# Performance work log

Measured on AMD Instinct MI355X. Metric: run time of the kernel, lower is better.

## Reference

```python
import jax, jax.numpy as jnp
import numpy as np

B, S, CL, DIM, HEADS, FFN = 2, 2048, 512, 2048, 16, 8192
EPS = 1e-6


def rms_norm(x, w):
    return x * jax.lax.rsqrt(jnp.mean(x * x, axis=-1, keepdims=True) + EPS) * w


def mha(q, k, v, num_heads):
    b, sq, d = q.shape
    sk = k.shape[1]
    hd = d // num_heads
    q = q.reshape(b, sq, num_heads, hd)
    k = k.reshape(b, sk, num_heads, hd)
    v = v.reshape(b, sk, num_heads, hd)
    attn = jnp.einsum('bqhd,bkhd->bhqk', q, k) * (hd ** -0.5)
    attn = jax.nn.softmax(attn, axis=-1)
    out = jnp.einsum('bhqk,bkhd->bqhd', attn, v)
    return out.reshape(b, sq, d)


def setup_inputs() -> dict:
    key = jax.random.key(0)
    ks = iter(jax.random.split(key, 48))
    nrm = lambda shape, scale: jax.random.normal(next(ks), shape, jnp.float32) * scale
    w_scale = DIM ** -0.5
    inp = {
        'x': nrm((B, S, DIM), 1.0),
        'e': nrm((B, 6, DIM), 0.5),
        'context': nrm((B, CL, DIM), 1.0),
        'modulation': nrm((1, 6, DIM), w_scale),
        'norm1_w': jnp.ones((DIM,), jnp.float32),
        'norm2_w': jnp.ones((DIM,), jnp.float32),
        'norm3_w': jnp.ones((DIM,), jnp.float32),
        'sa_nq_w': jnp.ones((DIM,), jnp.float32),
        'sa_nk_w': jnp.ones((DIM,), jnp.float32),
        'ffn_norm_w': jnp.ones((DIM,), jnp.float32),
        'sa_qw': nrm((DIM, DIM), w_scale), 'sa_qb': jnp.zeros((DIM,), jnp.float32),
        'sa_kw': nrm((DIM, DIM), w_scale), 'sa_kb': jnp.zeros((DIM,), jnp.float32),
        'sa_vw': nrm((DIM, DIM), w_scale), 'sa_vb': jnp.zeros((DIM,), jnp.float32),
        'sa_ow': nrm((DIM, DIM), w_scale), 'sa_ob': jnp.zeros((DIM,), jnp.float32),
        'ca_qw': nrm((DIM, DIM), w_scale), 'ca_qb': jnp.zeros((DIM,), jnp.float32),
        'ca_kw': nrm((DIM, DIM), w_scale), 'ca_kb': jnp.zeros((DIM,), jnp.float32),
        'ca_vw': nrm((DIM, DIM), w_scale), 'ca_vb': jnp.zeros((DIM,), jnp.float32),
        'ca_ow': nrm((DIM, DIM), w_scale), 'ca_ob': jnp.zeros((DIM,), jnp.float32),
        'ffn_w1': nrm((DIM, FFN), w_scale), 'ffn_b1': jnp.zeros((FFN,), jnp.float32),
        'ffn_w2': nrm((FFN, DIM), FFN ** -0.5), 'ffn_b2': jnp.zeros((DIM,), jnp.float32),
    }
    return inp


def reference(x, e, context, modulation, norm1_w, norm2_w, norm3_w, sa_nq_w, sa_nk_w,
              ffn_norm_w, sa_qw, sa_qb, sa_kw, sa_kb, sa_vw, sa_vb, sa_ow, sa_ob,
              ca_qw, ca_qb, ca_kw, ca_kb, ca_vw, ca_vb, ca_ow, ca_ob,
              ffn_w1, ffn_b1, ffn_w2, ffn_b2):
    # AdaLN modulation: (modulation + e) chunked into 6 along dim=1 -> each [B,1,DIM]
    mod = modulation + e
    e0, e1, e2, e3, e4, e5 = [mod[:, i:i + 1, :] for i in range(6)]

    # --- self attention with qk_norm=True ---
    h = rms_norm(x, norm1_w) * (1.0 + e1) + e0
    q = rms_norm(h @ sa_qw + sa_qb, sa_nq_w)
    k = rms_norm(h @ sa_kw + sa_kb, sa_nk_w)
    v = h @ sa_vw + sa_vb
    y = mha(q, k, v, HEADS) @ sa_ow + sa_ob
    x = x + y * e2

    # --- cross attention (cross_attn_norm=False, no qk norm) ---
    h = rms_norm(x, norm2_w)
    q = h @ ca_qw + ca_qb
    k = context @ ca_kw + ca_kb
    v = context @ ca_vw + ca_vb
    y = mha(q, k, v, HEADS) @ ca_ow + ca_ob
    x = x + y

    # --- FFN: modulate(norm3(x)) -> RMSNorm -> Linear -> GELU(tanh) -> Linear ---
    h = rms_norm(x, norm3_w) * (1.0 + e4) + e3
    h = rms_norm(h, ffn_norm_w)
    h = jax.nn.gelu(h @ ffn_w1 + ffn_b1, approximate=True)
    y = h @ ffn_w2 + ffn_b2
    x = x + y * e5
    return x
```

## Files before the change

### kernel.cpp

```cpp
#include <hip/hip_runtime.h>
#include <hip/hip_bf16.h>
#include <cstdint>

#define DIM   2048
#define HEADS 16
#define HD    128
#define SEQ   2048
#define CLEN  512
#define FFND  8192
#define BATCH 2

using bf16 = __hip_bfloat16;
typedef __attribute__((ext_vector_type(8))) short  short8;
typedef __attribute__((ext_vector_type(4))) short  short4v;
typedef __attribute__((ext_vector_type(4))) float  f32x4;
typedef __attribute__((ext_vector_type(8))) __bf16 bf16x8;

__device__ __forceinline__ short f2bs(float f){ bf16 h = __float2bfloat16(f); return __builtin_bit_cast(short, h); }
__device__ __forceinline__ float bs2f(short s){ return __builtin_bit_cast(float, (uint32_t)((uint16_t)s) << 16); }

__device__ __forceinline__ f32x4 mfma16(short8 a, short8 b, f32x4 c){
  return __builtin_amdgcn_mfma_f32_16x16x32_bf16(
      __builtin_bit_cast(bf16x8, a), __builtin_bit_cast(bf16x8, b), c, 0, 0, 0);
}

__device__ __forceinline__ void gload_lds16(const void* g, const void* l){
  __builtin_amdgcn_global_load_lds(
      (const __attribute__((address_space(1))) void*)(uintptr_t)g,
      (__attribute__((address_space(3))) void*)(uint32_t)(uintptr_t)l, 16, 0, 0);
}

__device__ __forceinline__ float block_sum(float v, float* sbuf, int tid){
  #pragma unroll
  for (int m = 32; m >= 1; m >>= 1) v += __shfl_xor(v, m, 64);
  const int w = tid >> 6;
  if ((tid & 63) == 0) sbuf[w] = v;
  __syncthreads();
  float r = sbuf[0] + sbuf[1] + sbuf[2] + sbuf[3];
  __syncthreads();
  return r;
}


__global__ void modadd_k(const float* __restrict__ m, const float* __restrict__ e,
                         float* __restrict__ out){
  int i = blockIdx.x * 256 + threadIdx.x;
  out[i] = m[i % (6 * DIM)] + e[i];
}

__global__ void f2b8_k(const float* __restrict__ in, bf16* __restrict__ out){
  int i = blockIdx.x * 256 + threadIdx.x;
  const float4* p = (const float4*)in;
  float4 a = p[2*i], c = p[2*i+1];
  short8 o;
  o[0]=f2bs(a.x); o[1]=f2bs(a.y); o[2]=f2bs(a.z); o[3]=f2bs(a.w);
  o[4]=f2bs(c.x); o[5]=f2bs(c.y); o[6]=f2bs(c.z); o[7]=f2bs(c.w);
  *((short8*)out + i) = o;
}

__global__ void biascat_k(const float* __restrict__ b0, const float* __restrict__ b1,
                          const float* __restrict__ b2, float* __restrict__ bcat){
  int i = blockIdx.x * 256 + threadIdx.x;
  const float* src = (i < DIM) ? b0 : (i < 2*DIM) ? b1 : b2;
  bcat[i] = src[i & (DIM-1)];
}

__global__ __launch_bounds__(256) void transpose_w(const float* __restrict__ W,
                                                   bf16* __restrict__ Wt, int K, int N){
  __shared__ float tile[32][33];
  const int tx = threadIdx.x & 31, ty = threadIdx.x >> 5;
  const size_t k0 = blockIdx.y * 32, n0 = blockIdx.x * 32;
  #pragma unroll
  for (int i = 0; i < 4; i++)
    tile[ty + i*8][tx] = W[(k0 + ty + i*8) * (size_t)N + n0 + tx];
  __syncthreads();
  #pragma unroll
  for (int i = 0; i < 4; i++)
    Wt[(n0 + ty + i*8) * (size_t)K + k0 + tx] = __float2bfloat16(tile[tx][ty + i*8]);
}

template<int MODE>
__global__ __launch_bounds__(256) void norm_x(const float* __restrict__ x,
    const float* __restrict__ w1, const float* __restrict__ w2,
    const float* __restrict__ mod, bf16* __restrict__ out, int S)
{
  const int row = blockIdx.x, tid = threadIdx.x;
  const int b = row / S;
  __shared__ float sbuf[4];
  const float* xr = x + (size_t)row * DIM;
  float v[8];
  #pragma unroll
  for (int i = 0; i < 2; i++){
    float4 t = *(const float4*)(xr + i*1024 + tid*4);
    v[i*4+0]=t.x; v[i*4+1]=t.y; v[i*4+2]=t.z; v[i*4+3]=t.w;
  }
  float ss = 0.f;
  #pragma unroll
  for (int j = 0; j < 8; j++) ss += v[j]*v[j];
  ss = block_sum(ss, sbuf, tid);
  const float r = rsqrtf(ss * (1.0f/DIM) + 1e-6f);
  const float* mb = mod + (size_t)b * 6 * DIM;
  float t8[8];
  #pragma unroll
  for (int i = 0; i < 2; i++)
    #pragma unroll
    for (int j = 0; j < 4; j++){
      int n = i*1024 + tid*4 + j;
      float val = v[i*4+j] * r * w1[n];
      if (MODE == 1) val = val * (1.f + mb[DIM + n]) + mb[n];
      if (MODE == 3) val = val * (1.f + mb[4*DIM + n]) + mb[3*DIM + n];
      t8[i*4+j] = val;
    }
  if (MODE == 3){
    float s2 = 0.f;
    #pragma unroll
    for (int j = 0; j < 8; j++) s2 += t8[j]*t8[j];
    s2 = block_sum(s2, sbuf, tid);
    const float r2 = rsqrtf(s2 * (1.0f/DIM) + 1e-6f);
    #pragma unroll
    for (int i = 0; i < 2; i++)
      #pragma unroll
      for (int j = 0; j < 4; j++){
        int n = i*1024 + tid*4 + j;
        t8[i*4+j] = t8[i*4+j] * r2 * w2[n];
      }
  }
  #pragma unroll
  for (int i = 0; i < 2; i++){
    short4v o;
    #pragma unroll
    for (int j = 0; j < 4; j++) o[j] = f2bs(t8[i*4+j]);
    *(short4v*)(out + (size_t)row*DIM + i*1024 + tid*4) = o;
  }
}

__global__ __launch_bounds__(256) void rmsnorm_bf16_ip(bf16* __restrict__ x,
                                                       const float* __restrict__ w){
  const int row = blockIdx.x, tid = threadIdx.x;
  __shared__ float sbuf[4];
  bf16* xr = x + (size_t)row * DIM;
  short8 v = *(const short8*)(xr + tid*8);
  float f[8]; float ss = 0.f;
  #pragma unroll
  for (int j = 0; j < 8; j++){ f[j] = bs2f(v[j]); ss += f[j]*f[j]; }
  ss = block_sum(ss, sbuf, tid);
  const float r = rsqrtf(ss * (1.0f/DIM) + 1e-6f);
  short8 o;
  #pragma unroll
  for (int j = 0; j < 8; j++) o[j] = f2bs(f[j] * r * w[tid*8 + j]);
  *(short8*)(xr + tid*8) = o;
}

template<int WM, int EPI>
__global__ __launch_bounds__(512) void gemm_v10(
    const bf16* __restrict__ A, const bf16* __restrict__ Bt,
    const float* __restrict__ bias, const float* __restrict__ xin,
    const float* __restrict__ mod, float* __restrict__ outf,
    bf16* __restrict__ outb, bf16* __restrict__ out1, bf16* __restrict__ out2,
    int M, int N, int K, int S_tok, int eidx)
{
  constexpr int WN  = 8 / WM;
  constexpr int BN  = WN * 64;
  constexpr int RPW = 256 / WM;
  constexpr int MI  = RPW / 16;
  constexpr int PH  = MI / 2;
  constexpr int ABYTES = 256 * 64 * 2;
  constexpr int BBYTES = BN * 64 * 2;
  constexpr int NBJ = BBYTES / 8192;

  __shared__ __align__(16) char lds[2][ABYTES + BBYTES];

  const int tid = threadIdx.x;
  const int w = tid >> 6, l = tid & 63;
  const int lrow = l & 15, lhi = l >> 4;
  const int wr = w / WN, wc = w % WN;
  const size_t m0 = (size_t)blockIdx.y * 256, n0 = (size_t)blockIdx.x * BN;

  f32x4 acc[MI][4] = {};

  const int srow = tid >> 3;
  const int sseg = (tid & 7) ^ (srow & 7);
  const bf16* gA[4]; const bf16* gB[NBJ];
  #pragma unroll
  for (int j = 0; j < 4; j++)   gA[j] = A  + (m0 + srow + 64*j) * (size_t)K + sseg*8;
  #pragma unroll
  for (int j = 0; j < NBJ; j++) gB[j] = Bt + (n0 + srow + 64*j) * (size_t)K + sseg*8;

  const int nt = K >> 6;

  {
    char* buf = lds[0];
    #pragma unroll
    for (int j = 0; j < 4; j++)   gload_lds16(gA[j], buf + (tid + j*512)*16);
    #pragma unroll
    for (int j = 0; j < NBJ; j++) gload_lds16(gB[j], buf + ABYTES + (tid + j*512)*16);
  }
  asm volatile("s_waitcnt vmcnt(0)" ::: "memory");
  __builtin_amdgcn_s_barrier();

  for (int t = 0; t < nt; ++t){
    const char* br = lds[t & 1];
    char* sb = lds[(t + 1) & 1];
    const bool dost = (t + 1 < nt);
    const size_t ko = (size_t)(t + 1) * 64;
    short8 bf[4];
    #pragma unroll
    for (int p = 0; p < PH; ++p){
      const int ks  = (MI == 8) ? (p >> 1) : p;
      const int mi0 = (MI == 8) ? (p & 1) * 4 : 0;
      const int seg = ((ks*4 + lhi) ^ (lrow & 7)) * 16;
      short8 af[4];
      #pragma unroll
      for (int i = 0; i < 4; i++){
        const int row = wr*RPW + (mi0 + i)*16 + lrow;
        af[i] = *(const short8*)(br + row*128 + seg);
      }
      if (MI == 4 || (p & 1) == 0){
        #pragma unroll
        for (int ni = 0; ni < 4; ni++){
          const int row = wc*64 + ni*16 + lrow;
          bf[ni] = *(const short8*)(br + ABYTES + row*128 + seg);
        }
      }
      if (dost){
        if (MI == 8){
          if (p == 0){
            #pragma unroll
            for (int j = 0; j < 4; j++)   gload_lds16(gA[j] + ko, sb + (tid + j*512)*16);
          } else if (p == 1){
            #pragma unroll
            for (int j = 0; j < NBJ; j++) gload_lds16(gB[j] + ko, sb + ABYTES + (tid + j*512)*16);
          }
        } else {
          if (p == 0){
            #pragma unroll
            for (int j = 0; j < 4; j++)   gload_lds16(gA[j] + ko, sb + (tid + j*512)*16);
            #pragma unroll
            for (int j = 0; j < NBJ; j++) gload_lds16(gB[j] + ko, sb + ABYTES + (tid + j*512)*16);
          }
        }
      }
      __builtin_amdgcn_sched_barrier(0);
      __builtin_amdgcn_s_barrier();
      asm volatile("s_waitcnt lgkmcnt(0)" ::: "memory");
      __builtin_amdgcn_sched_barrier(0);
      __builtin_amdgcn_s_setprio(1);
      #pragma unroll
      for (int i = 0; i < 4; i++)
        #pragma unroll
        for (int ni = 0; ni < 4; ni++)
          acc[mi0 + i][ni] = mfma16(af[i], bf[ni], acc[mi0 + i][ni]);
      __builtin_amdgcn_s_setprio(0);
      if (p == PH - 1){ asm volatile("s_waitcnt vmcnt(0)" ::: "memory"); }
      __builtin_amdgcn_sched_barrier(0);
      __builtin_amdgcn_s_barrier();
    }
  }

  #pragma unroll
  for (int mi = 0; mi < MI; mi++)
    #pragma unroll
    for (int ni = 0; ni < 4; ni++)
      #pragma unroll
      for (int r = 0; r < 4; r++){
        const size_t m = m0 + wr*RPW + mi*16 + lhi*4 + r;
        const size_t n = n0 + wc*64 + ni*16 + lrow;
        float v = acc[mi][ni][r] + bias[n];
        if constexpr (EPI == 0) {
          outb[m * N + n] = __float2bfloat16(v);
        } else if constexpr (EPI == 1) {
          const size_t b = m / S_tok, s = m % S_tok;
          const size_t h = n >> 7, d = n & 127;
          outb[((b*HEADS + h)*HD + d) * S_tok + s] = __float2bfloat16(v);
        } else if constexpr (EPI == 2) {
          const float ev = mod[(m / S_tok) * 6 * DIM + (size_t)eidx * DIM + n];
          outf[m * N + n] = xin[m * N + n] + v * ev;
        } else if constexpr (EPI == 3) {
          outf[m * N + n] += v;
        } else if constexpr (EPI == 4) {
          float u = 0.7978845608028654f * (v + 0.044715f * v * v * v);
          outb[m * N + n] = __float2bfloat16(0.5f * v * (1.0f + tanhf(u)));
        } else {
          const size_t sg = n >> 11, col = n & 2047;
          if (sg == 0)      outb[m * DIM + col] = __float2bfloat16(v);
          else if (sg == 1) out1[m * DIM + col] = __float2bfloat16(v);
          else {
            const size_t b = m / S_tok, s = m % S_tok;
            const size_t h = col >> 7, d = col & 127;
            out2[((b*HEADS + h)*HD + d) * S_tok + s] = __float2bfloat16(v);
          }
        }
      }
}

__global__ __launch_bounds__(256, 2) void attn_fwd(
    const bf16* __restrict__ Q, const bf16* __restrict__ Kp, const bf16* __restrict__ Vt,
    bf16* __restrict__ O, int SQ, int SKV)
{
  const int tid = threadIdx.x, w = tid >> 6, l = tid & 63;
  const int lrow = l & 15, lhi = l >> 4;
  const int nwg = gridDim.x;
  const int p = blockIdx.x;
  const int f = (p & 7) * (nwg >> 3) + (p >> 3);
  const int nqb = SQ >> 6;
  const int xq = f % nqb;
  const int h  = (f / nqb) % HEADS;
  const int b  = f / (nqb * HEADS);
  const int q0 = xq * 64 + w * 16;

  __shared__ __align__(16) char kls[2][16384];
  __shared__ __align__(16) char vls[2][16384];
  __shared__ __align__(16) bf16 P[4][16][72];
  const float scale = 0.08838834764831845f;

  const bf16* qp = Q + ((size_t)(b*SQ + q0 + lrow))*DIM + h*HD + lhi*8;
  short8 qf[4];
  #pragma unroll
  for (int ds = 0; ds < 4; ds++) qf[ds] = *(const short8*)(qp + ds*32);

  const bf16* kg = Kp + (size_t)b*SKV*DIM + h*HD;
  const bf16* vg = Vt + (size_t)(b*HEADS + h)*HD*SKV;

  f32x4 acc[8] = {};
  float m_run = -INFINITY, l_run = 0.f;
  const int nt = SKV >> 6;

  auto stage = [&](int buf, int kv0){
    char* kd = &kls[buf][0];
    #pragma unroll
    for (int i = 0; i < 4; i++){
      int sid = i*256 + tid;
      int row = sid >> 4, sg = sid & 15;
      int gsg = sg ^ (row & 7);
      gload_lds16(kg + (size_t)(kv0 + row)*DIM + gsg*8, kd + sid*16);
    }
    char* vd = &vls[buf][0];
    #pragma unroll
    for (int i = 0; i < 4; i++){
      int sid = i*256 + tid;
      int d = sid >> 3, sg = sid & 7;
      int gsg = sg ^ (d & 7);
      gload_lds16(vg + (size_t)d*SKV + kv0 + gsg*8, vd + sid*16);
    }
  };

  stage(0, 0);
  __syncthreads();

  for (int t = 0; t < nt; ++t){
    if (t + 1 < nt) stage((t + 1) & 1, (t + 1) * 64);
    const char* kb = &kls[t & 1][0];
    const char* vb = &vls[t & 1][0];

    f32x4 st[4] = {};
    #pragma unroll
    for (int kvf = 0; kvf < 4; kvf++){
      const int row = kvf*16 + lrow;
      const int rx = row & 7;
      #pragma unroll
      for (int ds = 0; ds < 4; ds++){
        const int seg = (ds*4 + lhi) ^ rx;
        short8 kf = *(const short8*)(kb + row*256 + seg*16);
        st[kvf] = mfma16(kf, qf[ds], st[kvf]);
      }
    }

    float sv[16]; float smax = -INFINITY;
    #pragma unroll
    for (int kvf = 0; kvf < 4; kvf++)
      #pragma unroll
      for (int r = 0; r < 4; r++){
        float xv = st[kvf][r] * scale;
        sv[kvf*4+r] = xv; smax = fmaxf(smax, xv);
      }
    smax = fmaxf(smax, __shfl_xor(smax, 16, 64));
    smax = fmaxf(smax, __shfl_xor(smax, 32, 64));
    const float mnew = fmaxf(m_run, smax);
    const float corr = __expf(m_run - mnew);
    float psum = 0.f;
    #pragma unroll
    for (int i = 0; i < 16; i++){ float pe = __expf(sv[i] - mnew); sv[i] = pe; psum += pe; }
    psum += __shfl_xor(psum, 16, 64); psum += __shfl_xor(psum, 32, 64);
    l_run = l_run * corr + psum;
    m_run = mnew;

    #pragma unroll
    for (int kvf = 0; kvf < 4; kvf++){
      short4v o;
      #pragma unroll
      for (int r = 0; r < 4; r++) o[r] = f2bs(sv[kvf*4+r]);
      *(short4v*)&P[w][lrow][kvf*16 + lhi*4] = o;
    }

    float cr[4];
    #pragma unroll
    for (int r = 0; r < 4; r++) cr[r] = __shfl(corr, lhi*4 + r, 64);
    #pragma unroll
    for (int df = 0; df < 8; df++){
      acc[df][0] *= cr[0]; acc[df][1] *= cr[1]; acc[df][2] *= cr[2]; acc[df][3] *= cr[3];
    }

    asm volatile("s_waitcnt lgkmcnt(0)" ::: "memory");
    __builtin_amdgcn_sched_barrier(0);

    short8 pf0 = *(const short8*)&P[w][lrow][lhi*8];
    short8 pf1 = *(const short8*)&P[w][lrow][32 + lhi*8];
    #pragma unroll
    for (int df = 0; df < 8; df++){
      const int d = df*16 + lrow;
      const int dx = d & 7;
      short8 vf0 = *(const short8*)(vb + d*128 + ((lhi)     ^ dx)*16);
      short8 vf1 = *(const short8*)(vb + d*128 + ((lhi + 4) ^ dx)*16);
      acc[df] = mfma16(pf0, vf0, acc[df]);
      acc[df] = mfma16(pf1, vf1, acc[df]);
    }
    __syncthreads();
  }

  const float linv = 1.0f / l_run;
  float li[4];
  #pragma unroll
  for (int r = 0; r < 4; r++) li[r] = __shfl(linv, lhi*4 + r, 64);
  #pragma unroll
  for (int df = 0; df < 8; df++)
    #pragma unroll
    for (int r = 0; r < 4; r++){
      const size_t q = q0 + lhi*4 + r;
      O[((size_t)(b*SQ + q))*DIM + h*HD + df*16 + lrow] = __float2bfloat16(acc[df][r] * li[r]);
    }
}


extern "C" void kernel_launch(void* const* d_in, const int* in_sizes, int n_in,
                              void* d_out, int out_size, void* d_ws, size_t ws_size,
                              hipStream_t stream)
{
  const float* x    = (const float*)d_in[0];
  const float* e    = (const float*)d_in[1];
  const float* ctx  = (const float*)d_in[2];
  const float* modw = (const float*)d_in[3];
  const float* n1w  = (const float*)d_in[4];
  const float* n2w  = (const float*)d_in[5];
  const float* n3w  = (const float*)d_in[6];
  const float* nqw  = (const float*)d_in[7];
  const float* nkw  = (const float*)d_in[8];
  const float* fnw  = (const float*)d_in[9];
  const float* saqw = (const float*)d_in[10]; const float* saqb = (const float*)d_in[11];
  const float* sakw = (const float*)d_in[12]; const float* sakb = (const float*)d_in[13];
  const float* savw = (const float*)d_in[14]; const float* savb = (const float*)d_in[15];
  const float* saow = (const float*)d_in[16]; const float* saob = (const float*)d_in[17];
  const float* caqw = (const float*)d_in[18]; const float* caqb = (const float*)d_in[19];
  const float* cakw = (const float*)d_in[20]; const float* cakb = (const float*)d_in[21];
  const float* cavw = (const float*)d_in[22]; const float* cavb = (const float*)d_in[23];
  const float* caow = (const float*)d_in[24]; const float* caob = (const float*)d_in[25];
  const float* fw1  = (const float*)d_in[26]; const float* fb1  = (const float*)d_in[27];
  const float* fw2  = (const float*)d_in[28]; const float* fb2  = (const float*)d_in[29];
  float* out = (float*)d_out;
  (void)in_sizes; (void)n_in; (void)out_size; (void)ws_size;

  char* ws = (char*)d_ws;
  size_t off = 0;
  auto alloc = [&](size_t bytes) -> void* {
    void* p = ws + off; off = (off + bytes + 255) & ~(size_t)255; return p;
  };
  bf16*  wt   = (bf16*)alloc((size_t)FFND * DIM * 2);
  float* mod  = (float*)alloc((size_t)BATCH * 6 * DIM * 4);
  float* bcat = (float*)alloc((size_t)3 * DIM * 4);
  bf16*  ctxb = (bf16*)alloc((size_t)BATCH * CLEN * DIM * 2);
  bf16*  hbuf = (bf16*)alloc((size_t)BATCH * SEQ * DIM * 2);
  bf16*  qbuf = (bf16*)alloc((size_t)BATCH * SEQ * DIM * 2);
  bf16*  kbuf = (bf16*)alloc((size_t)BATCH * SEQ * DIM * 2);
  bf16*  vtb  = (bf16*)alloc((size_t)BATCH * SEQ * DIM * 2);
  bf16*  aout = (bf16*)alloc((size_t)BATCH * SEQ * DIM * 2);
  float* xcur = (float*)alloc((size_t)BATCH * SEQ * DIM * 4);
  bf16*  hf   = (bf16*)alloc((size_t)BATCH * SEQ * FFND * 2);

  const int M = BATCH * SEQ;
  const int Mc = BATCH * CLEN;

  modadd_k<<<dim3(96), dim3(256), 0, stream>>>(modw, e, mod);
  f2b8_k<<<dim3(1024), dim3(256), 0, stream>>>(ctx, ctxb);
  biascat_k<<<dim3(24), dim3(256), 0, stream>>>(saqb, sakb, savb, bcat);

  norm_x<1><<<dim3(M), dim3(256), 0, stream>>>(x, n1w, nullptr, mod, hbuf, SEQ);

  transpose_w<<<dim3(DIM/32, DIM/32), dim3(256), 0, stream>>>(saqw, wt,                     DIM, DIM);
  transpose_w<<<dim3(DIM/32, DIM/32), dim3(256), 0, stream>>>(sakw, wt + (size_t)DIM*DIM,   DIM, DIM);
  transpose_w<<<dim3(DIM/32, DIM/32), dim3(256), 0, stream>>>(savw, wt + (size_t)2*DIM*DIM, DIM, DIM);
  gemm_v10<2,5><<<dim3(3*DIM/256, M/256), dim3(512), 0, stream>>>(hbuf, wt, bcat, nullptr, nullptr, nullptr, qbuf, kbuf, vtb, M, 3*DIM, DIM, SEQ, 0);
  rmsnorm_bf16_ip<<<dim3(M), dim3(256), 0, stream>>>(qbuf, nqw);
  rmsnorm_bf16_ip<<<dim3(M), dim3(256), 0, stream>>>(kbuf, nkw);

  attn_fwd<<<dim3((SEQ/64)*HEADS*BATCH), dim3(256), 0, stream>>>(qbuf, kbuf, vtb, aout, SEQ, SEQ);

  transpose_w<<<dim3(DIM/32, DIM/32), dim3(256), 0, stream>>>(saow, wt, DIM, DIM);
  gemm_v10<4,2><<<dim3(DIM/128, M/256), dim3(512), 0, stream>>>(aout, wt, saob, x, mod, xcur, nullptr, nullptr, nullptr, M, DIM, DIM, SEQ, 2);

  norm_x<2><<<dim3(M), dim3(256), 0, stream>>>(xcur, n2w, nullptr, mod, hbuf, SEQ);

  transpose_w<<<dim3(DIM/32, DIM/32), dim3(256), 0, stream>>>(caqw, wt, DIM, DIM);
  gemm_v10<4,0><<<dim3(DIM/128, M/256), dim3(512), 0, stream>>>(hbuf, wt, caqb, nullptr, nullptr, nullptr, qbuf, nullptr, nullptr, M, DIM, DIM, SEQ, 0);

  transpose_w<<<dim3(DIM/32, DIM/32), dim3(256), 0, stream>>>(cakw, wt, DIM, DIM);
  gemm_v10<4,0><<<dim3(DIM/128, Mc/256), dim3(512), 0, stream>>>(ctxb, wt, cakb, nullptr, nullptr, nullptr, kbuf, nullptr, nullptr, Mc, DIM, DIM, CLEN, 0);

  transpose_w<<<dim3(DIM/32, DIM/32), dim3(256), 0, stream>>>(cavw, wt, DIM, DIM);
  gemm_v10<4,1><<<dim3(DIM/128, Mc/256), dim3(512), 0, stream>>>(ctxb, wt, cavb, nullptr, nullptr, nullptr, vtb, nullptr, nullptr, Mc, DIM, DIM, CLEN, 0);

  attn_fwd<<<dim3((SEQ/64)*HEADS*BATCH), dim3(256), 0, stream>>>(qbuf, kbuf, vtb, aout, SEQ, CLEN);

  transpose_w<<<dim3(DIM/32, DIM/32), dim3(256), 0, stream>>>(caow, wt, DIM, DIM);
  gemm_v10<4,3><<<dim3(DIM/128, M/256), dim3(512), 0, stream>>>(aout, wt, caob, nullptr, nullptr, xcur, nullptr, nullptr, nullptr, M, DIM, DIM, SEQ, 0);

  norm_x<3><<<dim3(M), dim3(256), 0, stream>>>(xcur, n3w, fnw, mod, hbuf, SEQ);

  transpose_w<<<dim3(FFND/32, DIM/32), dim3(256), 0, stream>>>(fw1, wt, DIM, FFND);
  gemm_v10<2,4><<<dim3(FFND/256, M/256), dim3(512), 0, stream>>>(hbuf, wt, fb1, nullptr, nullptr, nullptr, hf, nullptr, nullptr, M, FFND, DIM, SEQ, 0);

  transpose_w<<<dim3(DIM/32, FFND/32), dim3(256), 0, stream>>>(fw2, wt, FFND, DIM);
  gemm_v10<4,2><<<dim3(DIM/128, M/256), dim3(512), 0, stream>>>(hf, wt, fb2, xcur, mod, out, nullptr, nullptr, nullptr, M, DIM, FFND, SEQ, 5);
}
```

Measured before the change: 994.0 us.

## Rework GEMM to triple-buffered LDS pipeline with new tile configs

Replaces the double-buffered GEMM with a three-stage LDS ring that prefetches two K-tiles ahead and waits on partial vmcnt counts rather than draining all loads. It adds two tile configurations: 256x256 with BK=32 for the wide QKV and FFN1 GEMMs, and 128x256 with BK=64 for the N=2048 GEMMs. The swizzle patterns change to match each BK. The aim is to hide more global-memory latency behind MFMA work. The cost is more LDS per block, which may lower occupancy, and the 128-row tiles give a different grid shape.

```diff
diff --git a/kernel.cpp b/kernel.cpp
--- a/kernel.cpp
+++ b/kernel.cpp
@@ -151,93 +151,125 @@
   *(short8*)(xr + tid*8) = o;
 }
 
-template<int WM, int EPI>
-__global__ __launch_bounds__(512) void gemm_v10(
+template<int CFG, int EPI>
+__global__ __launch_bounds__(512) void gemm_v11(
     const bf16* __restrict__ A, const bf16* __restrict__ Bt,
     const float* __restrict__ bias, const float* __restrict__ xin,
     const float* __restrict__ mod, float* __restrict__ outf,
     bf16* __restrict__ outb, bf16* __restrict__ out1, bf16* __restrict__ out2,
     int M, int N, int K, int S_tok, int eidx)
 {
-  constexpr int WN  = 8 / WM;
-  constexpr int BN  = WN * 64;
-  constexpr int RPW = 256 / WM;
+  constexpr int BM  = (CFG == 0) ? 256 : 128;
+  constexpr int BK  = (CFG == 0) ? 32 : 64;
+  constexpr int RPW = BM / 2;
   constexpr int MI  = RPW / 16;
-  constexpr int PH  = MI / 2;
-  constexpr int ABYTES = 256 * 64 * 2;
-  constexpr int BBYTES = BN * 64 * 2;
-  constexpr int NBJ = BBYTES / 8192;
-
-  __shared__ __align__(16) char lds[2][ABYTES + BBYTES];
+  constexpr int KS  = BK / 32;
+  constexpr int RB  = BK * 2;
+  constexpr int ABY = BM * RB;
+  constexpr int BBY = 256 * RB;
+  constexpr int NLA = ABY / 8192;
+  constexpr int NLB = BBY / 8192;
+  constexpr int SEGS = BK / 8;
+
+  __shared__ __align__(16) char lds[3][ABY + BBY];
 
   const int tid = threadIdx.x;
   const int w = tid >> 6, l = tid & 63;
   const int lrow = l & 15, lhi = l >> 4;
-  const int wr = w / WN, wc = w % WN;
-  const size_t m0 = (size_t)blockIdx.y * 256, n0 = (size_t)blockIdx.x * BN;
+  const int wr = w >> 2, wc = w & 3;
+  const size_t m0 = (size_t)blockIdx.y * BM, n0 = (size_t)blockIdx.x * 256;
 
   f32x4 acc[MI][4] = {};
 
-  const int srow = tid >> 3;
-  const int sseg = (tid & 7) ^ (srow & 7);
-  const bf16* gA[4]; const bf16* gB[NBJ];
-  #pragma unroll
-  for (int j = 0; j < 4; j++)   gA[j] = A  + (m0 + srow + 64*j) * (size_t)K + sseg*8;
-  #pragma unroll
-  for (int j = 0; j < NBJ; j++) gB[j] = Bt + (n0 + srow + 64*j) * (size_t)K + sseg*8;
-
-  const int nt = K >> 6;
-
-  {
-    char* buf = lds[0];
-    #pragma unroll
-    for (int j = 0; j < 4; j++)   gload_lds16(gA[j], buf + (tid + j*512)*16);
-    #pragma unroll
-    for (int j = 0; j < NBJ; j++) gload_lds16(gB[j], buf + ABYTES + (tid + j*512)*16);
-  }
-  asm volatile("s_waitcnt vmcnt(0)" ::: "memory");
+  const bf16* gA[NLA]; const bf16* gB[NLB];
+  #pragma unroll
+  for (int j = 0; j < NLA; j++){
+    const int s = tid + j*512, row = s / SEGS, ps = s % SEGS;
+    const int gs = (CFG == 0) ? (ps ^ ((row >> 1) & 3)) : (ps ^ (row & 7));
+    gA[j] = A + (m0 + row) * (size_t)K + gs*8;
+  }
+  #pragma unroll
+  for (int j = 0; j < NLB; j++){
+    const int s = tid + j*512, row = s / SEGS, ps = s % SEGS;
+    const int gs = (CFG == 0) ? (ps ^ ((row >> 1) & 3)) : (ps ^ (row & 7));
+    gB[j] = Bt + (n0 + row) * (size_t)K + gs*8;
+  }
+
+  const int nt = K / BK;
+
+  auto stageA = [&](int kt, char* buf){
+    const size_t ko = (size_t)kt * BK;
+    #pragma unroll
+    for (int j = 0; j < NLA; j++) gload_lds16(gA[j] + ko, buf + (tid + j*512)*16);
+  };
+  auto stageB = [&](int kt, char* buf, int jj){
+    const size_t ko = (size_t)kt * BK;
+    gload_lds16(gB[jj] + ko, buf + ABY + (tid + jj*512)*16);
+  };
+
+  stageA(0, lds[0]);
+  #pragma unroll
+  for (int j = 0; j < NLB; j++) stageB(0, lds[0], j);
+  stageA(1, lds[1]);
+  #pragma unroll
+  for (int j = 0; j < NLB; j++) stageB(1, lds[1], j);
+  if constexpr (CFG == 0) { asm volatile("s_waitcnt vmcnt(4)" ::: "memory"); }
+  else                    { asm volatile("s_waitcnt vmcnt(6)" ::: "memory"); }
   __builtin_amdgcn_s_barrier();
 
+  const int rswzA = (CFG == 0) ? ((lrow >> 1) & 3) : (lrow & 7);
+
+  int bi = 0;
   for (int t = 0; t < nt; ++t){
-    const char* br = lds[t & 1];
-    char* sb = lds[(t + 1) & 1];
-    const bool dost = (t + 1 < nt);
-    const size_t ko = (size_t)(t + 1) * 64;
-    short8 bf[4];
-    #pragma unroll
-    for (int p = 0; p < PH; ++p){
-      const int ks  = (MI == 8) ? (p >> 1) : p;
-      const int mi0 = (MI == 8) ? (p & 1) * 4 : 0;
-      const int seg = ((ks*4 + lhi) ^ (lrow & 7)) * 16;
-      short8 af[4];
-      #pragma unroll
-      for (int i = 0; i < 4; i++){
-        const int row = wr*RPW + (mi0 + i)*16 + lrow;
-        af[i] = *(const short8*)(br + row*128 + seg);
-      }
-      if (MI == 4 || (p & 1) == 0){
+    const char* br = lds[bi];
+    int wi = bi + 2; if (wi >= 3) wi -= 3;
+    char* sb = lds[wi];
+    const bool dost = (t + 2 < nt);
+
+    short8 bf[4*KS];
+    #pragma unroll
+    for (int p = 0; p < 2; ++p){
+      short8 af[2*KS == 2 ? 4 : 4];
+      if constexpr (CFG == 0){
+        const int mi0 = p * 4;
         #pragma unroll
-        for (int ni = 0; ni < 4; ni++){
-          const int row = wc*64 + ni*16 + lrow;
-          bf[ni] = *(const short8*)(br + ABYTES + row*128 + seg);
+        for (int i = 0; i < 4; i++){
+          const int row = wr*RPW + (mi0 + i)*16 + lrow;
+          af[i] = *(const short8*)(br + row*RB + ((lhi ^ rswzA))*16);
         }
+        if (p == 0){
+          #pragma unroll
+          for (int ni = 0; ni < 4; ni++){
+            const int row = wc*64 + ni*16 + lrow;
+            bf[ni] = *(const short8*)(br + ABY + row*RB + ((lhi ^ rswzA))*16);
+          }
+        }
+      } else {
+        const int mi0 = p * 2;
+        #pragma unroll
+        for (int i = 0; i < 2; i++)
+          #pragma unroll
+          for (int ks = 0; ks < 2; ks++){
+            const int row = wr*RPW + (mi0 + i)*16 + lrow;
+            af[i*2+ks] = *(const short8*)(br + row*RB + (((ks*4 + lhi) ^ rswzA))*16);
+          }
+        if (p == 0){
+          #pragma unroll
+          for (int ni = 0; ni < 4; ni++)
+            #pragma unroll
+            for (int ks = 0; ks < 2; ks++){
+              const int row = wc*64 + ni*16 + lrow;
+              bf[ni*2+ks] = *(const short8*)(br + ABY + row*RB + (((ks*4 + lhi) ^ rswzA))*16);
+            }
+        }
       }
       if (dost){
-        if (MI == 8){
-          if (p == 0){
-            #pragma unroll
-            for (int j = 0; j < 4; j++)   gload_lds16(gA[j] + ko, sb + (tid + j*512)*16);
-          } else if (p == 1){
-            #pragma unroll
-            for (int j = 0; j < NBJ; j++) gload_lds16(gB[j] + ko, sb + ABYTES + (tid + j*512)*16);
-          }
+        if constexpr (CFG == 0){
+          if (p == 0) stageA(t + 2, sb);
+          else { stageB(t + 2, sb, 0); stageB(t + 2, sb, 1); }
         } else {
-          if (p == 0){
-            #pragma unroll
-            for (int j = 0; j < 4; j++)   gload_lds16(gA[j] + ko, sb + (tid + j*512)*16);
-            #pragma unroll
-            for (int j = 0; j < NBJ; j++) gload_lds16(gB[j] + ko, sb + ABYTES + (tid + j*512)*16);
-          }
+          if (p == 0){ stageA(t + 2, sb); stageB(t + 2, sb, 0); }
+          else { stageB(t + 2, sb, 1); stageB(t + 2, sb, 2); stageB(t + 2, sb, 3); }
         }
       }
       __builtin_amdgcn_sched_barrier(0);
@@ -245,16 +277,34 @@
       asm volatile("s_waitcnt lgkmcnt(0)" ::: "memory");
       __builtin_amdgcn_sched_barrier(0);
       __builtin_amdgcn_s_setprio(1);
-      #pragma unroll
-      for (int i = 0; i < 4; i++)
+      if constexpr (CFG == 0){
+        const int mi0 = p * 4;
         #pragma unroll
-        for (int ni = 0; ni < 4; ni++)
-          acc[mi0 + i][ni] = mfma16(af[i], bf[ni], acc[mi0 + i][ni]);
+        for (int i = 0; i < 4; i++)
+          #pragma unroll
+          for (int ni = 0; ni < 4; ni++)
+            acc[mi0 + i][ni] = mfma16(af[i], bf[ni], acc[mi0 + i][ni]);
+      } else {
+        const int mi0 = p * 2;
+        #pragma unroll
+        for (int i = 0; i < 2; i++)
+          #pragma unroll
+          for (int ni = 0; ni < 4; ni++)
+            #pragma unroll
+            for (int ks = 0; ks < 2; ks++)
+              acc[mi0 + i][ni] = mfma16(af[i*2+ks], bf[ni*2+ks], acc[mi0 + i][ni]);
+      }
       __builtin_amdgcn_s_setprio(0);
-      if (p == PH - 1){ asm volatile("s_waitcnt vmcnt(0)" ::: "memory"); }
+      if (p == 1){
+        if (dost){
+          if constexpr (CFG == 0) { asm volatile("s_waitcnt vmcnt(4)" ::: "memory"); }
+          else                    { asm volatile("s_waitcnt vmcnt(6)" ::: "memory"); }
+        } else if (t + 1 < nt)    { asm volatile("s_waitcnt vmcnt(0)" ::: "memory"); }
+      }
       __builtin_amdgcn_sched_barrier(0);
       __builtin_amdgcn_s_barrier();
     }
+    bi = (bi + 1 == 3) ? 0 : bi + 1;
   }
 
   #pragma unroll
@@ -487,36 +537,36 @@
   transpose_w<<<dim3(DIM/32, DIM/32), dim3(256), 0, stream>>>(saqw, wt,                     DIM, DIM);
   transpose_w<<<dim3(DIM/32, DIM/32), dim3(256), 0, stream>>>(sakw, wt + (size_t)DIM*DIM,   DIM, DIM);
   transpose_w<<<dim3(DIM/32, DIM/32), dim3(256), 0, stream>>>(savw, wt + (size_t)2*DIM*DIM, DIM, DIM);
-  gemm_v10<2,5><<<dim3(3*DIM/256, M/256), dim3(512), 0, stream>>>(hbuf, wt, bcat, nullptr, nullptr, nullptr, qbuf, kbuf, vtb, M, 3*DIM, DIM, SEQ, 0);
+  gemm_v11<0,5><<<dim3(3*DIM/256, M/256), dim3(512), 0, stream>>>(hbuf, wt, bcat, nullptr, nullptr, nullptr, qbuf, kbuf, vtb, M, 3*DIM, DIM, SEQ, 0);
   rmsnorm_bf16_ip<<<dim3(M), dim3(256), 0, stream>>>(qbuf, nqw);
   rmsnorm_bf16_ip<<<dim3(M), dim3(256), 0, stream>>>(kbuf, nkw);
 
   attn_fwd<<<dim3((SEQ/64)*HEADS*BATCH), dim3(256), 0, stream>>>(qbuf, kbuf, vtb, aout, SEQ, SEQ);
 
   transpose_w<<<dim3(DIM/32, DIM/32), dim3(256), 0, stream>>>(saow, wt, DIM, DIM);
-  gemm_v10<4,2><<<dim3(DIM/128, M/256), dim3(512), 0, stream>>>(aout, wt, saob, x, mod, xcur, nullptr, nullptr, nullptr, M, DIM, DIM, SEQ, 2);
+  gemm_v11<1,2><<<dim3(DIM/256, M/128), dim3(512), 0, stream>>>(aout, wt, saob, x, mod, xcur, nullptr, nullptr, nullptr, M, DIM, DIM, SEQ, 2);
 
   norm_x<2><<<dim3(M), dim3(256), 0, stream>>>(xcur, n2w, nullptr, mod, hbuf, SEQ);
 
   transpose_w<<<dim3(DIM/32, DIM/32), dim3(256), 0, stream>>>(caqw, wt, DIM, DIM);
-  gemm_v10<4,0><<<dim3(DIM/128, M/256), dim3(512), 0, stream>>>(hbuf, wt, caqb, nullptr, nullptr, nullptr, qbuf, nullptr, nullptr, M, DIM, DIM, SEQ, 0);
+  gemm_v11<1,0><<<dim3(DIM/256, M/128), dim3(512), 0, stream>>>(hbuf, wt, caqb, nullptr, nullptr, nullptr, qbuf, nullptr, nullptr, M, DIM, DIM, SEQ, 0);
 
   transpose_w<<<dim3(DIM/32, DIM/32), dim3(256), 0, stream>>>(cakw, wt, DIM, DIM);
-  gemm_v10<4,0><<<dim3(DIM/128, Mc/256), dim3(512), 0, stream>>>(ctxb, wt, cakb, nullptr, nullptr, nullptr, kbuf, nullptr, nullptr, Mc, DIM, DIM, CLEN, 0);
+  gemm_v11<1,0><<<dim3(DIM/256, Mc/128), dim3(512), 0, stream>>>(ctxb, wt, cakb, nullptr, nullptr, nullptr, kbuf, nullptr, nullptr, Mc, DIM, DIM, CLEN, 0);
 
   transpose_w<<<dim3(DIM/32, DIM/32), dim3(256), 0, stream>>>(cavw, wt, DIM, DIM);
-  gemm_v10<4,1><<<dim3(DIM/128, Mc/256), dim3(512), 0, stream>>>(ctxb, wt, cavb, nullptr, nullptr, nullptr, vtb, nullptr, nullptr, Mc, DIM, DIM, CLEN, 0);
+  gemm_v11<1,1><<<dim3(DIM/256, Mc/128), dim3(512), 0, stream>>>(ctxb, wt, cavb, nullptr, nullptr, nullptr, vtb, nullptr, nullptr, Mc, DIM, DIM, CLEN, 0);
 
   attn_fwd<<<dim3((SEQ/64)*HEADS*BATCH), dim3(256), 0, stream>>>(qbuf, kbuf, vtb, aout, SEQ, CLEN);
 
   transpose_w<<<dim3(DIM/32, DIM/32), dim3(256), 0, stream>>>(caow, wt, DIM, DIM);
-  gemm_v10<4,3><<<dim3(DIM/128, M/256), dim3(512), 0, stream>>>(aout, wt, caob, nullptr, nullptr, xcur, nullptr, nullptr, nullptr, M, DIM, DIM, SEQ, 0);
+  gemm_v11<1,3><<<dim3(DIM/256, M/128), dim3(512), 0, stream>>>(aout, wt, caob, nullptr, nullptr, xcur, nullptr, nullptr, nullptr, M, DIM, DIM, SEQ, 0);
 
   norm_x<3><<<dim3(M), dim3(256), 0, stream>>>(xcur, n3w, fnw, mod, hbuf, SEQ);
 
   transpose_w<<<dim3(FFND/32, DIM/32), dim3(256), 0, stream>>>(fw1, wt, DIM, FFND);
-  gemm_v10<2,4><<<dim3(FFND/256, M/256), dim3(512), 0, stream>>>(hbuf, wt, fb1, nullptr, nullptr, nullptr, hf, nullptr, nullptr, M, FFND, DIM, SEQ, 0);
+  gemm_v11<0,4><<<dim3(FFND/256, M/256), dim3(512), 0, stream>>>(hbuf, wt, fb1, nullptr, nullptr, nullptr, hf, nullptr, nullptr, M, FFND, DIM, SEQ, 0);
 
   transpose_w<<<dim3(DIM/32, FFND/32), dim3(256), 0, stream>>>(fw2, wt, FFND, DIM);
-  gemm_v10<4,2><<<dim3(DIM/128, M/256), dim3(512), 0, stream>>>(hf, wt, fb2, xcur, mod, out, nullptr, nullptr, nullptr, M, DIM, FFND, SEQ, 5);
-}
+  gemm_v11<1,2><<<dim3(DIM/256, M/128), dim3(512), 0, stream>>>(hf, wt, fb2, xcur, mod, out, nullptr, nullptr, nullptr, M, DIM, FFND, SEQ, 5);
+}
```

After: 989.5 us. Within noise of the previous version (-0.5%).
